# Kernel tuning notes

Measured on AMD Instinct MI355X. Metric: run time of the kernel, lower is better.

## Reference

```python
import jax, jax.numpy as jnp
import numpy as np

MIN_EXPERT_CAPACITY = 4
CAPACITY_FACTOR = 1.0


def setup_inputs() -> dict:
    key = jax.random.key(0)
    k0, k1, k2, k3 = jax.random.split(key, 4)
    B, S, D, E, F = 4, 2048, 1024, 8, 4096
    x = jax.random.normal(k0, (B, S, D), dtype=jnp.float32)
    router_w = jax.random.normal(k1, (D, E), dtype=jnp.float32) * (D ** -0.5)
    w1 = jax.random.normal(k2, (E, D, F), dtype=jnp.float32) * (D ** -0.5)
    b1 = jnp.zeros((E, F), dtype=jnp.float32)
    w2 = jax.random.normal(k3, (E, F, D), dtype=jnp.float32) * (F ** -0.5)
    b2 = jnp.zeros((E, D), dtype=jnp.float32)
    return {"x": x, "router_w": router_w, "w1": w1, "b1": b1, "w2": w2, "b2": b2}


def _moe_forward(x, router_w, w1, b1, w2, b2):
    B, S, D = x.shape
    E = router_w.shape[1]
    G = 1  # num_groups (single device -> all-to-all is identity)
    T = B * S  # tokens per group
    C = max(int(round(CAPACITY_FACTOR * T / E)), MIN_EXPERT_CAPACITY)

    xt = x.reshape(G, T, D)
    # ---- top-1 tokens-choose masked router ----
    logits = jnp.einsum('gtd,de->gte', xt, router_w)
    probs = jax.nn.softmax(logits, axis=-1)
    gate = jnp.max(probs, axis=-1)          # [g, t]
    idx = jnp.argmax(probs, axis=-1)        # [g, t]
    emask = jax.nn.one_hot(idx, E, dtype=x.dtype)  # [g, t, e]
    # position of each token within its chosen expert's buffer (0-based);
    # -1 for unselected slots -> one_hot gives zeros
    pos = jnp.cumsum(emask, axis=1) * emask - 1.0
    pos = pos.astype(jnp.int32)
    # drop tokens beyond capacity
    slot = jax.nn.one_hot(pos, C, dtype=x.dtype)   # [g, t, e, c]
    dispatch = emask[..., None] * slot             # [g, t, e, c] (0/1)
    combine = dispatch * gate[..., None, None]     # [g, t, e, c]

    # ---- dispatch / expert FFN / combine ----
    expert_inputs = jnp.einsum('gtd,gtec->gecd', xt, dispatch)        # [g, e, c, d]
    h = jax.nn.relu(jnp.einsum('gecd,edf->gecf', expert_inputs, w1) + b1[None, :, None, :])
    expert_outputs = jnp.einsum('gecf,efd->gecd', h, w2) + b2[None, :, None, :]
    out = jnp.einsum('gecd,gtec->gtd', expert_outputs, combine)       # [g, t, d]
    return out.reshape(B, S, D)


def reference(x, router_w, w1, b1, w2, b2):
    return _moe_forward(x, router_w, w1, b1, w2, b2)
```

## Files before the change

### kernel.cpp

```cpp
#include <hip/hip_runtime.h>
#include <hip/hip_fp16.h>

typedef unsigned short ushort_t;
typedef __attribute__((ext_vector_type(8))) _Float16 half8v;
typedef __attribute__((ext_vector_type(4))) float float4v;
typedef __attribute__((ext_vector_type(8))) unsigned short ushort8v;

#define DEV_INLINE __device__ __forceinline__

DEV_INLINE ushort_t f2h_bits(float f) {
  return __half_as_ushort(__float2half(f));
}

__global__ __launch_bounds__(256) void router_kernel(
    const float* __restrict__ x, const float* __restrict__ rw,
    int* __restrict__ idx, float* __restrict__ gate)
{
  constexpr int D = 1024, E = 8;
  int token = (int)((blockIdx.x * 256 + threadIdx.x) >> 6);
  int lane = threadIdx.x & 63;
  const float* xr = x + (size_t)token * D;
  float acc[E];
#pragma unroll
  for (int e = 0; e < E; ++e) acc[e] = 0.f;
  for (int d = lane; d < D; d += 64) {
    float xv = xr[d];
#pragma unroll
    for (int e = 0; e < E; ++e) acc[e] += xv * rw[d * E + e];
  }
#pragma unroll
  for (int off = 32; off >= 1; off >>= 1) {
#pragma unroll
    for (int e = 0; e < E; ++e) acc[e] += __shfl_xor(acc[e], off);
  }
  if (lane == 0) {
    float m = acc[0]; int am = 0;
#pragma unroll
    for (int e = 1; e < E; ++e) { if (acc[e] > m) { m = acc[e]; am = e; } }
    float s = 0.f;
#pragma unroll
    for (int e = 0; e < E; ++e) s += __expf(acc[e] - m);
    idx[token] = am;
    gate[token] = 1.0f / s;
  }
}

__global__ __launch_bounds__(1024) void scan_kernel(
    const int* __restrict__ idx,
    int* __restrict__ slotmap, int* __restrict__ tok2slot)
{
  constexpr int C = 1024, E = 8;
  __shared__ unsigned long long s0[1024];
  __shared__ unsigned long long s1[1024];
  int tid = threadIdx.x;
  int myidx[8];
  unsigned long long c0 = 0, c1 = 0;
#pragma unroll
  for (int j = 0; j < 8; ++j) {
    int e = idx[tid * 8 + j];
    myidx[j] = e;
    if (e < 4) c0 += 1ull << (16 * e);
    else       c1 += 1ull << (16 * (e - 4));
  }
  s0[tid] = c0; s1[tid] = c1;
  __syncthreads();
  for (int off = 1; off < 1024; off <<= 1) {
    unsigned long long b0 = 0, b1 = 0;
    if (tid >= off) { b0 = s0[tid - off]; b1 = s1[tid - off]; }
    __syncthreads();
    s0[tid] += b0; s1[tid] += b1;
    __syncthreads();
  }
  unsigned long long p0 = s0[tid] - c0, p1 = s1[tid] - c1;
  unsigned long long t0 = s0[1023], t1 = s1[1023];
  int cnt[E];
#pragma unroll
  for (int e = 0; e < 4; ++e) {
    cnt[e]     = (int)((p0 >> (16 * e)) & 0xFFFF);
    cnt[4 + e] = (int)((p1 >> (16 * e)) & 0xFFFF);
  }
#pragma unroll
  for (int j = 0; j < 8; ++j) {
    int t = tid * 8 + j;
    int e = myidx[j];
    int pos = cnt[e]++;
    if (pos < C) {
      slotmap[e * C + pos] = t;
      tok2slot[t] = e * C + pos;
    } else {
      tok2slot[t] = -1;
    }
  }
  int total[E];
#pragma unroll
  for (int e = 0; e < 4; ++e) {
    total[e]     = (int)((t0 >> (16 * e)) & 0xFFFF);
    total[4 + e] = (int)((t1 >> (16 * e)) & 0xFFFF);
  }
  for (int s = tid; s < E * C; s += 1024) {
    int e = s / C, c = s % C;
    if (c >= total[e]) slotmap[s] = -1;
  }
}

__global__ __launch_bounds__(256) void gather_kernel(
    const float* __restrict__ x, const int* __restrict__ slotmap,
    ushort_t* __restrict__ Xe)
{
  constexpr int D = 1024;
  int slot = blockIdx.x;
  int t = slotmap[slot];
  int tid = threadIdx.x;
  ushort4* dst = (ushort4*)(Xe + (size_t)slot * D);
  ushort4 o;
  if (t >= 0) {
    float4 v = ((const float4*)(x + (size_t)t * D))[tid];
    o.x = f2h_bits(v.x); o.y = f2h_bits(v.y); o.z = f2h_bits(v.z); o.w = f2h_bits(v.w);
  } else {
    o.x = 0; o.y = 0; o.z = 0; o.w = 0;
  }
  dst[tid] = o;
}

__global__ __launch_bounds__(256) void transpose_cvt2(
    const float* __restrict__ w1, ushort_t* __restrict__ w1t,
    const float* __restrict__ w2, ushort_t* __restrict__ w2t)
{
  __shared__ ushort_t tile[64][65];
  int bb = blockIdx.x;
  const float* in; ushort_t* out; int R, Cc, bx, by, bz;
  if (bb < 8192) {
    in = w1; out = w1t; R = 1024; Cc = 4096;
    bz = bb >> 10; int rr = bb & 1023; bx = rr & 63; by = rr >> 6;
  } else {
    bb -= 8192;
    in = w2; out = w2t; R = 4096; Cc = 1024;
    bz = bb >> 10; int rr = bb & 1023; bx = rr & 15; by = rr >> 4;
  }
  size_t base = (size_t)bz * (size_t)R * (size_t)Cc;
  int c0 = bx * 64, r0 = by * 64;
  int tx = threadIdx.x & 63, ty = threadIdx.x >> 6;
#pragma unroll
  for (int i = 0; i < 16; ++i) {
    int r = ty + 4 * i;
    tile[r][tx] = f2h_bits(in[base + (size_t)(r0 + r) * Cc + c0 + tx]);
  }
  __syncthreads();
#pragma unroll
  for (int i = 0; i < 2; ++i) {
    int chunk = (int)threadIdx.x + i * 256;
    int c = chunk >> 3, g = chunk & 7;
    ushort8v v;
#pragma unroll
    for (int j = 0; j < 8; ++j) v[j] = tile[8 * g + j][c];
    *(ushort8v*)(out + base + (size_t)(c0 + c) * R + r0 + 8 * g) = v;
  }
}

__global__ __launch_bounds__(256) void combine_kernel(
    const float* __restrict__ p, const float* __restrict__ b2,
    const int* __restrict__ tok2slot, const float* __restrict__ gate,
    float* __restrict__ out)
{
  constexpr int D = 1024;
  constexpr size_t ECD = (size_t)8 * 1024 * 1024;
  int t = blockIdx.x;
  int d4 = threadIdx.x;
  float4* o = (float4*)(out + (size_t)t * D);
  int slot = tok2slot[t];
  if (slot < 0) { o[d4] = make_float4(0.f, 0.f, 0.f, 0.f); return; }
  int e = slot >> 10;
  float g = gate[t];
  float4 a = ((const float4*)(p + (size_t)slot * D))[d4];
  float4 b = ((const float4*)(p + ECD + (size_t)slot * D))[d4];
  float4 bb = ((const float4*)(b2 + (size_t)e * D))[d4];
  o[d4] = make_float4((a.x + b.x + bb.x) * g, (a.y + b.y + bb.y) * g,
                      (a.z + b.z + bb.z) * g, (a.w + b.w + bb.w) * g);
}

#define BAR()   asm volatile("s_barrier" ::: "memory")
#define LGKM0() asm volatile("s_waitcnt lgkmcnt(0)" ::: "memory")
#define VM4()   asm volatile("s_waitcnt vmcnt(4)" ::: "memory")
#define VM6()   asm volatile("s_waitcnt vmcnt(6)" ::: "memory")
#define VM0()   asm volatile("s_waitcnt vmcnt(0)" ::: "memory")

#define RD_A0(buf) { _Pragma("unroll") for (int i_ = 0; i_ < 4; ++i_) { \
  _Pragma("unroll") for (int kh_ = 0; kh_ < 2; ++kh_) \
    aS0[i_][kh_] = *(const half8v*)&lds[buf][kh_*KH + (arow + i_*16)*32 + axor]; } }
#define RD_A1(buf) { _Pragma("unroll") for (int i_ = 0; i_ < 4; ++i_) { \
  _Pragma("unroll") for (int kh_ = 0; kh_ < 2; ++kh_) \
    aS1[i_][kh_] = *(const half8v*)&lds[buf][kh_*KH + (arow + (4+i_)*16)*32 + axor]; } }
#define RD_B0(buf) { _Pragma("unroll") for (int j_ = 0; j_ < 2; ++j_) { \
  _Pragma("unroll") for (int kh_ = 0; kh_ < 2; ++kh_) \
    bS0[j_][kh_] = *(const half8v*)&lds[buf][AELEM + kh_*KH + (brow + j_*16)*32 + axor]; } }
#define RD_B1(buf) { _Pragma("unroll") for (int j_ = 0; j_ < 2; ++j_) { \
  _Pragma("unroll") for (int kh_ = 0; kh_ < 2; ++kh_) \
    bS1[j_][kh_] = *(const half8v*)&lds[buf][AELEM + kh_*KH + (brow + (2+j_)*16)*32 + axor]; } }

#define MQ(AS, BS, MB, NB) { __builtin_amdgcn_s_setprio(1); \
  _Pragma("unroll") for (int i_ = 0; i_ < 4; ++i_) { \
  _Pragma("unroll") for (int j_ = 0; j_ < 2; ++j_) { \
    acc[(MB)+i_][(NB)+j_] = __builtin_amdgcn_mfma_f32_16x16x32_f16(AS[i_][0], BS[j_][0], acc[(MB)+i_][(NB)+j_], 0, 0, 0); \
    acc[(MB)+i_][(NB)+j_] = __builtin_amdgcn_mfma_f32_16x16x32_f16(AS[i_][1], BS[j_][1], acc[(MB)+i_][(NB)+j_], 0, 0, 0); } } \
  __builtin_amdgcn_s_setprio(0); }

template<int KFULL, int NTM, int NTN, int SK, int MODE>
__global__ __launch_bounds__(512, 2) void gemm8p(
    const ushort_t* __restrict__ A, const ushort_t* __restrict__ Bt,
    const float* __restrict__ bias,
    ushort_t* __restrict__ Hout, float* __restrict__ outp)
{
  constexpr int M_ = NTM * 256, N_ = NTN * 256;
  constexpr int KB = KFULL / SK;
  constexpr int NT = KB / 64;
  constexpr int NU = NT / 2;
  constexpr int KH = 256 * 32;
  constexpr int AELEM = 2 * KH;
  constexpr int WPB = NTM * NTN * SK;
  constexpr int NWG = 8 * WPB;
  constexpr int CPX = NWG / 8;

  __shared__ __attribute__((aligned(16))) ushort_t lds[2][2 * AELEM];

  const int bid = blockIdx.x;
  const int swz = (bid & 7) * CPX + (bid >> 3);
  const int e   = swz / WPB;
  int r = swz % WPB;
  const int sk  = r / (NTM * NTN);  r %= NTM * NTN;
  const int nt  = r / NTM;
  const int mt  = r % NTM;
  const int kb0 = sk * KB;

  const ushort_t* Ae = A  + (size_t)e * M_ * KFULL + (size_t)(mt * 256) * KFULL + kb0;
  const ushort_t* Be = Bt + (size_t)e * N_ * KFULL + (size_t)(nt * 256) * KFULL + kb0;

  const int tid  = threadIdx.x;
  const int lane = tid & 63;
  const int w    = tid >> 6;
  const int wr   = w >> 2;
  const int wc   = w & 3;
  const int l15  = lane & 15;
  const int axor = ((lane >> 4) ^ ((l15 >> 1) & 3)) << 3;
  const int arow = wr * 128 + l15;
  const int brow = wc * 64 + l15;

  const int srow = tid >> 2;
  const int su   = tid & 3;
  auto stage = [&](int buf, int isB, int h, int ktile) {
    const ushort_t* base = isB ? Be : Ae;
#pragma unroll
    for (int kh = 0; kh < 2; ++kh) {
      int row = h * 128 + srow;
      int ul  = su ^ ((row >> 1) & 3);
      const ushort_t* src = base + (size_t)row * KFULL + ktile * 64 + kh * 32 + ul * 8;
      __builtin_amdgcn_global_load_lds(
          (const __attribute__((address_space(1))) void*)src,
          (__attribute__((address_space(3))) void*)(&lds[buf][isB * AELEM + kh * KH + h * 4096 + tid * 8]),
          16, 0, 0);
    }
  };

  float4v acc[8][4] = {};
  half8v aS0[4][2], aS1[4][2], bS0[2][2], bS1[2][2];

  stage(0, 0, 0, 0); stage(0, 0, 1, 0); stage(0, 1, 0, 0); stage(0, 1, 1, 0);
  stage(1, 0, 0, 1); stage(1, 0, 1, 1); stage(1, 1, 0, 1);
  VM6(); BAR();
  RD_B0(0); RD_A0(0);

  for (int u = 0; u < NU - 1; ++u) {
    const int t1 = 2 * u + 1, t2 = 2 * u + 2, t3 = 2 * u + 3;
    RD_B1(0); RD_A1(0); stage(1, 1, 1, t1);
    BAR(); MQ(aS0, bS0, 0, 0); LGKM0(); BAR();
    stage(0, 0, 0, t2);
    BAR(); MQ(aS0, bS1, 0, 2); BAR();
    stage(0, 0, 1, t2);
    BAR(); MQ(aS1, bS0, 4, 0); VM4(); BAR();
    RD_B0(1); RD_A0(1); stage(0, 1, 0, t2);
    BAR(); MQ(aS1, bS1, 4, 2); BAR();
    RD_B1(1); RD_A1(1); stage(0, 1, 1, t2);
    BAR(); MQ(aS0, bS0, 0, 0); LGKM0(); BAR();
    stage(1, 0, 0, t3);
    BAR(); MQ(aS0, bS1, 0, 2); BAR();
    stage(1, 0, 1, t3);
    BAR(); MQ(aS1, bS0, 4, 0); VM4(); BAR();
    RD_B0(0); RD_A0(0); stage(1, 1, 0, t3);
    BAR(); MQ(aS1, bS1, 4, 2); BAR();
  }
  {
    RD_B1(0); RD_A1(0); stage(1, 1, 1, NT - 1);
    BAR(); MQ(aS0, bS0, 0, 0); LGKM0(); BAR();
    BAR(); MQ(aS0, bS1, 0, 2); BAR();
    BAR(); MQ(aS1, bS0, 4, 0); VM0(); BAR();
    RD_B0(1); RD_A0(1);
    BAR(); MQ(aS1, bS1, 4, 2); BAR();
    RD_B1(1); RD_A1(1);
    BAR(); MQ(aS0, bS0, 0, 0); BAR();
    BAR(); MQ(aS0, bS1, 0, 2); BAR();
    BAR(); MQ(aS1, bS0, 4, 0); BAR();
    MQ(aS1, bS1, 4, 2);
  }

  const int lr4   = (lane >> 4) * 4;
  const int mbase = mt * 256 + wr * 128;
  const int nbase = nt * 256 + wc * 64;

  if (MODE == 0) {
    float bv[4];
#pragma unroll
    for (int j = 0; j < 4; ++j) bv[j] = bias[e * N_ + nbase + j * 16 + l15];
    ushort_t* He = Hout + (size_t)e * M_ * N_;
#pragma unroll
    for (int i = 0; i < 8; ++i) {
#pragma unroll
      for (int q = 0; q < 4; ++q) {
        int m = mbase + i * 16 + lr4 + q;
#pragma unroll
        for (int j = 0; j < 4; ++j) {
          float v = acc[i][j][q] + bv[j];
          v = v > 0.f ? v : 0.f;
          He[(size_t)m * N_ + nbase + j * 16 + l15] = f2h_bits(v);
        }
      }
    }
  } else {
    float* pe = outp + ((size_t)(sk * 8 + e)) * (size_t)M_ * N_;
#pragma unroll
    for (int i = 0; i < 8; ++i) {
#pragma unroll
      for (int q = 0; q < 4; ++q) {
        int m = mbase + i * 16 + lr4 + q;
#pragma unroll
        for (int j = 0; j < 4; ++j) {
          pe[(size_t)m * N_ + nbase + j * 16 + l15] = acc[i][j][q];
        }
      }
    }
  }
}

extern "C" void kernel_launch(void* const* d_in, const int* in_sizes, int n_in,
                              void* d_out, int out_size, void* d_ws, size_t ws_size,
                              hipStream_t stream)
{
  const float* x  = (const float*)d_in[0];
  const float* rw = (const float*)d_in[1];
  const float* w1 = (const float*)d_in[2];
  const float* b1 = (const float*)d_in[3];
  const float* w2 = (const float*)d_in[4];
  const float* b2 = (const float*)d_in[5];
  float* out = (float*)d_out;

  constexpr int D = 1024, E = 8, F = 4096, T = 8192, C = 1024;

  char* p = (char*)d_ws;
  auto take = [&](size_t bytes) { char* r = p; p += (bytes + 255) & ~(size_t)255; return r; };
  ushort_t* w1t = (ushort_t*)take((size_t)E * D * F * 2);
  ushort_t* w2t = (ushort_t*)take((size_t)E * F * D * 2);
  ushort_t* Xe  = (ushort_t*)take((size_t)E * C * D * 2);
  ushort_t* H   = (ushort_t*)take((size_t)E * C * F * 2);
  int*      idx = (int*)take((size_t)T * 4);
  float*   gate = (float*)take((size_t)T * 4);
  int*  slotmap = (int*)take((size_t)E * C * 4);
  int* tok2slot = (int*)take((size_t)T * 4);

  float* partials = (float*)w1t;

  router_kernel<<<T / 4, 256, 0, stream>>>(x, rw, idx, gate);
  scan_kernel<<<1, 1024, 0, stream>>>(idx, slotmap, tok2slot);
  gather_kernel<<<E * C, 256, 0, stream>>>(x, slotmap, Xe);
  transpose_cvt2<<<16384, 256, 0, stream>>>(w1, w1t, w2, w2t);
  gemm8p<1024, 4, 16, 1, 0><<<512, 512, 0, stream>>>(Xe, w1t, b1, H, nullptr);
  gemm8p<4096, 4, 4, 2, 1><<<256, 512, 0, stream>>>(H, w2t, nullptr, nullptr, partials);
  combine_kernel<<<T, 256, 0, stream>>>(partials, b2, tok2slot, gate, out);
}
```

Before: 277.6 us.

## Fuse router into weight transpose kernel with larger 1024x32 transpose tiles

Merges the router kernel and the fp32-to-fp16 weight transpose into one launch, giving the router blocks first and the transpose blocks after them. The transpose now uses 1024x32 tiles with float4 loads and 16-byte stores of whole 1024-element output rows, which replaces the small 64x64 tiles and cuts the block count. This removes one launch and lets the router work overlap with the bandwidth-bound weight conversion. In exchange each block needs about 72KB of shared memory, which lowers occupancy and also applies to the router blocks.

```diff
diff --git a/kernel.cpp b/kernel.cpp
--- a/kernel.cpp
+++ b/kernel.cpp
@@ -12,36 +12,81 @@
   return __half_as_ushort(__float2half(f));
 }
 
-__global__ __launch_bounds__(256) void router_kernel(
+__global__ __launch_bounds__(256) void fused_rt(
     const float* __restrict__ x, const float* __restrict__ rw,
-    int* __restrict__ idx, float* __restrict__ gate)
-{
-  constexpr int D = 1024, E = 8;
-  int token = (int)((blockIdx.x * 256 + threadIdx.x) >> 6);
-  int lane = threadIdx.x & 63;
-  const float* xr = x + (size_t)token * D;
-  float acc[E];
-#pragma unroll
-  for (int e = 0; e < E; ++e) acc[e] = 0.f;
-  for (int d = lane; d < D; d += 64) {
-    float xv = xr[d];
-#pragma unroll
-    for (int e = 0; e < E; ++e) acc[e] += xv * rw[d * E + e];
-  }
-#pragma unroll
-  for (int off = 32; off >= 1; off >>= 1) {
-#pragma unroll
-    for (int e = 0; e < E; ++e) acc[e] += __shfl_xor(acc[e], off);
-  }
-  if (lane == 0) {
-    float m = acc[0]; int am = 0;
-#pragma unroll
-    for (int e = 1; e < E; ++e) { if (acc[e] > m) { m = acc[e]; am = e; } }
-    float s = 0.f;
-#pragma unroll
-    for (int e = 0; e < E; ++e) s += __expf(acc[e] - m);
-    idx[token] = am;
-    gate[token] = 1.0f / s;
+    int* __restrict__ idx, float* __restrict__ gate,
+    const float* __restrict__ w1, ushort_t* __restrict__ w1t,
+    const float* __restrict__ w2, ushort_t* __restrict__ w2t)
+{
+  __shared__ ushort_t lt[1024][36];
+  int bb = blockIdx.x;
+  const int tid = threadIdx.x;
+  if (bb < 2048) {
+    constexpr int D = 1024, E = 8;
+    int token = (bb * 256 + tid) >> 6;
+    int lane = tid & 63;
+    const float* xr = x + (size_t)token * D;
+    float acc[E];
+#pragma unroll
+    for (int e = 0; e < E; ++e) acc[e] = 0.f;
+    for (int d = lane; d < D; d += 64) {
+      float xv = xr[d];
+#pragma unroll
+      for (int e = 0; e < E; ++e) acc[e] += xv * rw[d * E + e];
+    }
+#pragma unroll
+    for (int off = 32; off >= 1; off >>= 1) {
+#pragma unroll
+      for (int e = 0; e < E; ++e) acc[e] += __shfl_xor(acc[e], off);
+    }
+    if (lane == 0) {
+      float m = acc[0]; int am = 0;
+#pragma unroll
+      for (int e = 1; e < E; ++e) { if (acc[e] > m) { m = acc[e]; am = e; } }
+      float s = 0.f;
+#pragma unroll
+      for (int e = 0; e < E; ++e) s += __expf(acc[e] - m);
+      idx[token] = am;
+      gate[token] = 1.0f / s;
+    }
+    return;
+  }
+  bb -= 2048;
+  const float* inp; ushort_t* outp; int Cc, R2;
+  if (bb < 1024) {
+    int e = bb >> 7, ct = bb & 127;
+    Cc = 4096; R2 = 1024;
+    inp  = w1 + (size_t)e * 1024 * 4096 + ct * 32;
+    outp = w1t + (size_t)e * 4096 * 1024 + (size_t)(ct * 32) * 1024;
+  } else {
+    bb -= 1024;
+    int e = bb >> 7, rr = bb & 127;
+    int rt = rr >> 5, ct = rr & 31;
+    Cc = 1024; R2 = 4096;
+    inp  = w2 + (size_t)e * 4096 * 1024 + (size_t)(rt * 1024) * 1024 + ct * 32;
+    outp = w2t + (size_t)e * 1024 * 4096 + (size_t)(ct * 32) * 4096 + rt * 1024;
+  }
+  const int pr  = tid >> 3;
+  const int pc4 = (tid & 7) * 4;
+#pragma unroll
+  for (int p = 0; p < 32; ++p) {
+    int r = p * 32 + pr;
+    float4 v = *(const float4*)&inp[(size_t)r * Cc + pc4];
+    ushort4 o4;
+    o4.x = f2h_bits(v.x); o4.y = f2h_bits(v.y);
+    o4.z = f2h_bits(v.z); o4.w = f2h_bits(v.w);
+    *(ushort4*)&lt[r][pc4] = o4;
+  }
+  __syncthreads();
+  const int j2    = tid >> 7;
+  const int chunk = tid & 127;
+#pragma unroll
+  for (int p = 0; p < 16; ++p) {
+    int j = p * 2 + j2;
+    ushort8v o;
+#pragma unroll
+    for (int i = 0; i < 8; ++i) o[i] = lt[chunk * 8 + i][j];
+    *(ushort8v*)&outp[(size_t)j * R2 + chunk * 8] = o;
   }
 }
 
@@ -120,41 +165,6 @@
     o.x = 0; o.y = 0; o.z = 0; o.w = 0;
   }
   dst[tid] = o;
-}
-
-__global__ __launch_bounds__(256) void transpose_cvt2(
-    const float* __restrict__ w1, ushort_t* __restrict__ w1t,
-    const float* __restrict__ w2, ushort_t* __restrict__ w2t)
-{
-  __shared__ ushort_t tile[64][65];
-  int bb = blockIdx.x;
-  const float* in; ushort_t* out; int R, Cc, bx, by, bz;
-  if (bb < 8192) {
-    in = w1; out = w1t; R = 1024; Cc = 4096;
-    bz = bb >> 10; int rr = bb & 1023; bx = rr & 63; by = rr >> 6;
-  } else {
-    bb -= 8192;
-    in = w2; out = w2t; R = 4096; Cc = 1024;
-    bz = bb >> 10; int rr = bb & 1023; bx = rr & 15; by = rr >> 4;
-  }
-  size_t base = (size_t)bz * (size_t)R * (size_t)Cc;
-  int c0 = bx * 64, r0 = by * 64;
-  int tx = threadIdx.x & 63, ty = threadIdx.x >> 6;
-#pragma unroll
-  for (int i = 0; i < 16; ++i) {
-    int r = ty + 4 * i;
-    tile[r][tx] = f2h_bits(in[base + (size_t)(r0 + r) * Cc + c0 + tx]);
-  }
-  __syncthreads();
-#pragma unroll
-  for (int i = 0; i < 2; ++i) {
-    int chunk = (int)threadIdx.x + i * 256;
-    int c = chunk >> 3, g = chunk & 7;
-    ushort8v v;
-#pragma unroll
-    for (int j = 0; j < 8; ++j) v[j] = tile[8 * g + j][c];
-    *(ushort8v*)(out + base + (size_t)(c0 + c) * R + r0 + 8 * g) = v;
-  }
 }
 
 __global__ __launch_bounds__(256) void combine_kernel(
@@ -366,10 +376,9 @@
 
   float* partials = (float*)w1t;
 
-  router_kernel<<<T / 4, 256, 0, stream>>>(x, rw, idx, gate);
+  fused_rt<<<4096, 256, 0, stream>>>(x, rw, idx, gate, w1, w1t, w2, w2t);
   scan_kernel<<<1, 1024, 0, stream>>>(idx, slotmap, tok2slot);
   gather_kernel<<<E * C, 256, 0, stream>>>(x, slotmap, Xe);
-  transpose_cvt2<<<16384, 256, 0, stream>>>(w1, w1t, w2, w2t);
   gemm8p<1024, 4, 16, 1, 0><<<512, 512, 0, stream>>>(Xe, w1t, b1, H, nullptr);
   gemm8p<4096, 4, 4, 2, 1><<<256, 512, 0, stream>>>(H, w2t, nullptr, nullptr, partials);
   combine_kernel<<<T, 256, 0, stream>>>(partials, b2, tok2slot, gate, out);
```

Measured after the change: 311.3 us. 12.1% more time.
